# Optimization experiments

Measured on AMD Instinct MI355X. Metric: run time of the kernel, lower is better.

The kernel has to match this reference:

```python
import jax, jax.numpy as jnp
import numpy as np

STATE_DIM = 128
N_RBF = 20
R_CUT = 10.0
N_NODES = 25000
N_EDGES = 250000
N_GRAPHS = 512
N_ATOMS = 100
NUM_ROUNDS = 1


def setup_inputs() -> dict:
    key = jax.random.key(0)
    ks = jax.random.split(key, 20)
    D = STATE_DIM

    def w(k, shape, s=0.05):
        return jax.random.normal(k, shape, jnp.float32) * s

    return {
        "edge_vec": jax.random.normal(ks[0], (N_EDGES, 3), jnp.float32),
        "embedding": w(ks[1], (N_ATOMS, D), 1.0),
        "phi_W1": w(ks[2], (D, D)), "phi_b1": jnp.zeros((D,), jnp.float32),
        "phi_W2": w(ks[3], (D, 3 * D)), "phi_b2": jnp.zeros((3 * D,), jnp.float32),
        "filt_W": w(ks[4], (N_RBF, 3 * D)), "filt_b": jnp.zeros((3 * D,), jnp.float32),
        "upd_W1": w(ks[5], (2 * D, D)), "upd_b1": jnp.zeros((D,), jnp.float32),
        "upd_W2": w(ks[6], (D, 3 * D)), "upd_b2": jnp.zeros((3 * D,), jnp.float32),
        "out_W1": w(ks[7], (D, D)), "out_b1": jnp.zeros((D,), jnp.float32),
        "out_W2": w(ks[8], (D, 1)), "out_b2": jnp.zeros((1,), jnp.float32),
        "U_W": w(ks[9], (D, D)),
        "V_W": w(ks[10], (D, D)),
        "atom_types": jax.random.randint(ks[11], (N_NODES,), 0, N_ATOMS),
        "node_from": jax.random.randint(ks[12], (N_EDGES,), 0, N_NODES),
        "node_to": jax.random.randint(ks[13], (N_EDGES,), 0, N_NODES),
        "node_graph_index": jnp.sort(jax.random.randint(ks[14], (N_NODES,), 0, N_GRAPHS)),
        "num_graphs": N_GRAPHS,
    }


def _painn_forward(edge_vec, embedding, phi_W1, phi_b1, phi_W2, phi_b2,
                   filt_W, filt_b, upd_W1, upd_b1, upd_W2, upd_b2,
                   out_W1, out_b1, out_W2, out_b2, U_W, V_W,
                   atom_types, node_from, node_to, node_graph_index, num_graphs):
    silu = jax.nn.silu
    D = STATE_DIM
    # initial node scalar states from atom-type embedding; vector states zero
    state = embedding[atom_types]                         # [N, D]
    state_vec = jnp.zeros((state.shape[0], 3, D), state.dtype)  # [N, 3, D]

    # edge geometry (constant across rounds)
    d = jnp.linalg.norm(edge_vec, axis=1, keepdims=True)  # [E, 1]
    kfreq = jnp.arange(1, N_RBF + 1, dtype=jnp.float32)   # PaiNN sinc radial basis
    rbf = jnp.sin(kfreq * jnp.pi * d / R_CUT) / d         # [E, n]
    fc = 0.5 * (jnp.cos(jnp.pi * d / R_CUT) + 1.0) * (d < R_CUT)  # cosine cutoff [E,1]
    W_out = (rbf @ filt_W + filt_b) * fc                  # [E, 3D]
    normalized = edge_vec / d                             # [E, 3]

    for _ in range(NUM_ROUNDS):
        # --- message block ---
        inp = state[node_from]                             # gather [E, D]
        phi = silu(inp @ phi_W1 + phi_b1) @ phi_W2 + phi_b2  # [E, 3D]
        pf = phi * W_out                                   # [E, 3D]
        m1, m2, m3 = pf[:, :D], pf[:, D:2 * D], pf[:, 2 * D:]
        msg_vec = (state_vec[node_from] * m1[:, None, :]
                   + normalized[:, :, None] * m3[:, None, :])  # [E, 3, D]
        state = state.at[node_to].add(m2)                  # scatter-add scalars
        state_vec = state_vec.at[node_to].add(msg_vec)     # scatter-add vectors

        # --- update block (torch detaches state_vec here) ---
        sv = jax.lax.stop_gradient(state_vec)
        Up = sv @ U_W                                      # [N, 3, D]
        Vp = sv @ V_W                                      # [N, 3, D]
        UV = jnp.sum(Up * Vp, axis=1)                      # [N, D]
        Vn = jnp.linalg.norm(Vp, axis=1)                   # [N, D]
        h = jnp.concatenate([Vn, state], axis=1)           # [N, 2D]
        a = silu(h @ upd_W1 + upd_b1) @ upd_W2 + upd_b2    # [N, 3D]
        a_vv, a_sv, a_ss = a[:, :D], a[:, D:2 * D], a[:, 2 * D:]
        state = state + a_ss + UV * a_sv
        state_vec = state_vec + Up * a_vv[:, None, :]

    idx = node_graph_index - node_graph_index[0]
    graph_state = jax.ops.segment_sum(state, idx, num_segments=num_graphs)  # [G, D]
    return silu(graph_state @ out_W1 + out_b1) @ out_W2 + out_b2            # [G, 1]


def reference(edge_vec, embedding, phi_W1, phi_b1, phi_W2, phi_b2,
              filt_W, filt_b, upd_W1, upd_b1, upd_W2, upd_b2,
              out_W1, out_b1, out_W2, out_b2, U_W, V_W,
              atom_types, node_from, node_to, node_graph_index, num_graphs):
    return _painn_forward(edge_vec, embedding, phi_W1, phi_b1, phi_W2, phi_b2,
                          filt_W, filt_b, upd_W1, upd_b1, upd_W2, upd_b2,
                          out_W1, out_b1, out_W2, out_b2, U_W, V_W,
                          atom_types, node_from, node_to, node_graph_index, num_graphs)
```

## Files before the change

### kernel.cpp

```cpp
#include <hip/hip_runtime.h>
#include <math.h>

#define D 128
#define NRBF 20
#define NEDGES 250000
#define NNODES 25000
#define NGRAPHS 512
#define NATOMS 100

constexpr float RCUT = 10.0f;
constexpr float PI_F = 3.14159265358979323846f;

__device__ __forceinline__ float silu_f(float x) { return x / (1.0f + __expf(-x)); }

__global__ __launch_bounds__(128) void k_phi_table(
    const float* __restrict__ emb, const float* __restrict__ W1, const float* __restrict__ b1,
    const float* __restrict__ W2, const float* __restrict__ b2, float* __restrict__ phi_tab)
{
    __shared__ float s_in[D];
    __shared__ float s_hid[D];
    const int t = blockIdx.x;
    const int j = threadIdx.x;
    s_in[j] = emb[t * D + j];
    __syncthreads();
    float acc = b1[j];
    for (int c = 0; c < D; ++c) acc = fmaf(s_in[c], W1[c * D + j], acc);
    s_hid[j] = silu_f(acc);
    __syncthreads();
    #pragma unroll
    for (int r = 0; r < 3; ++r) {
        const int col = r * D + j;
        float a2 = b2[col];
        for (int c = 0; c < D; ++c) a2 = fmaf(s_hid[c], W2[c * 384 + col], a2);
        phi_tab[t * 384 + col] = a2;
    }
}

__global__ void k_zero(int* __restrict__ counts, float* __restrict__ gs)
{
    const int i = blockIdx.x * 256 + threadIdx.x;
    if (i < NNODES) counts[i] = 0;
    if (i < NGRAPHS * D) gs[i] = 0.f;
}

__global__ void k_hist(const int* __restrict__ node_to, int* __restrict__ counts)
{
    const int e = blockIdx.x * 256 + threadIdx.x;
    if (e < NEDGES) atomicAdd(&counts[node_to[e]], 1);
}

__global__ __launch_bounds__(1024) void k_scan(int* __restrict__ counts,
                                               int* __restrict__ row_ptr)
{
    __shared__ int s[1024];
    const int t = threadIdx.x;
    const int base = t * 25;
    int sum = 0;
    for (int j = 0; j < 25; ++j) {
        const int idx = base + j;
        if (idx < NNODES) sum += counts[idx];
    }
    s[t] = sum;
    __syncthreads();
    for (int off = 1; off < 1024; off <<= 1) {
        int v = 0;
        if (t >= off) v = s[t - off];
        __syncthreads();
        if (t >= off) s[t] += v;
        __syncthreads();
    }
    int run = (t > 0) ? s[t - 1] : 0;
    for (int j = 0; j < 25; ++j) {
        const int idx = base + j;
        if (idx < NNODES) {
            const int v = counts[idx];
            row_ptr[idx] = run;
            counts[idx] = run;
            run += v;
        }
    }
    if (t == 1023) row_ptr[NNODES] = s[1023];
}

__global__ __launch_bounds__(256) void k_pre(
    const float* __restrict__ edge_vec, const int* __restrict__ node_from,
    const int* __restrict__ node_to, const int* __restrict__ atom_types,
    int* __restrict__ cursor, float* __restrict__ edata, int* __restrict__ ety)
{
    const int e = blockIdx.x * 256 + threadIdx.x;
    if (e >= NEDGES) return;
    const float x = edge_vec[e * 3 + 0];
    const float y = edge_vec[e * 3 + 1];
    const float z = edge_vec[e * 3 + 2];
    const float d = sqrtf(x * x + y * y + z * z);
    const float inv = 1.0f / d;
    const float th = PI_F * d / RCUT;
    const float fc = (d < RCUT) ? 0.5f * (__cosf(th) + 1.0f) : 0.0f;
    const float sc = fc * inv;

    float buf[24];
    #pragma unroll
    for (int k = 0; k < NRBF; ++k) buf[k] = __sinf((float)(k + 1) * th) * sc;
    buf[20] = fc;
    buf[21] = x * inv;
    buf[22] = y * inv;
    buf[23] = z * inv;

    const int slot = atomicAdd(&cursor[node_to[e]], 1);
    float* o = edata + (size_t)slot * 24;
    #pragma unroll
    for (int q = 0; q < 6; ++q) *(float4*)(o + q * 4) = *(float4*)&buf[q * 4];
    ety[slot] = atom_types[node_from[e]];
}

#define GNPB 16
#define CHUNK 64
__global__ __launch_bounds__(256, 4) void k_gather(
    const int* __restrict__ row_ptr, const float* __restrict__ edata,
    const int* __restrict__ ety, const float* __restrict__ phi_tab,
    const float* __restrict__ filt_W, const float* __restrict__ filt_b,
    const float* __restrict__ emb, const int* __restrict__ atom_types,
    float* __restrict__ state, float* __restrict__ sv)
{
    __shared__ __align__(16) float s_ed[CHUNK * 24];
    __shared__ int s_ep[CHUNK];
    __shared__ int s_rp[GNPB + 1];

    const int t = threadIdx.x;
    const bool is_m2 = (t < 128);
    const int lane = t & 127;
    const int c = is_m2 ? (128 + lane) : (256 + lane);

    const int n0 = blockIdx.x * GNPB;
    const int nEnd = min(n0 + GNPB, NNODES);

    if (t <= GNPB) s_rp[t] = row_ptr[min(n0 + t, NNODES)];

    float fw[NRBF];
    #pragma unroll
    for (int k = 0; k < NRBF; ++k) fw[k] = filt_W[k * 384 + c];
    const float fb = filt_b[c];

    __syncthreads();
    const int e0 = s_rp[0];
    const int e1 = s_rp[nEnd - n0];

    int cur = n0;
    int nb = s_rp[1];
    float a0 = 0.f, a1 = 0.f, a2 = 0.f;

    auto do_edge = [&](int j) {
        const float4* p = (const float4*)(s_ed + j * 24);
        const float4 q0 = p[0], q1 = p[1], q2 = p[2], q3 = p[3], q4 = p[4], q5 = p[5];
        const float pt = phi_tab[s_ep[j] * 384 + c];
        float wa = fb * q5.x;
        float wb = q2.z * fw[10];
        wa = fmaf(q0.x, fw[0], wa);  wb = fmaf(q2.w, fw[11], wb);
        wa = fmaf(q0.y, fw[1], wa);  wb = fmaf(q3.x, fw[12], wb);
        wa = fmaf(q0.z, fw[2], wa);  wb = fmaf(q3.y, fw[13], wb);
        wa = fmaf(q0.w, fw[3], wa);  wb = fmaf(q3.z, fw[14], wb);
        wa = fmaf(q1.x, fw[4], wa);  wb = fmaf(q3.w, fw[15], wb);
        wa = fmaf(q1.y, fw[5], wa);  wb = fmaf(q4.x, fw[16], wb);
        wa = fmaf(q1.z, fw[6], wa);  wb = fmaf(q4.y, fw[17], wb);
        wa = fmaf(q1.w, fw[7], wa);  wb = fmaf(q4.z, fw[18], wb);
        wa = fmaf(q2.x, fw[8], wa);  wb = fmaf(q4.w, fw[19], wb);
        wa = fmaf(q2.y, fw[9], wa);
        const float pf = pt * (wa + wb);
        if (is_m2) {
            a0 += pf;
        } else {
            a0 = fmaf(q5.y, pf, a0);
            a1 = fmaf(q5.z, pf, a1);
            a2 = fmaf(q5.w, pf, a2);
        }
    };

    auto flush = [&]() {
        if (is_m2) {
            state[cur * D + lane] = emb[atom_types[cur] * D + lane] + a0;
        } else {
            float* b = sv + (size_t)cur * 3 * D + lane;
            b[0] = a0; b[128] = a1; b[256] = a2;
        }
        a0 = a1 = a2 = 0.f;
        ++cur;
        nb = s_rp[cur - n0 + 1];
    };

    for (int base = e0; base < e1; base += CHUNK) {
        const int cnt = min(CHUNK, e1 - base);
        __syncthreads();
        for (int i = t; i < cnt * 6; i += 256)
            ((float4*)s_ed)[i] = ((const float4*)edata)[(size_t)base * 6 + i];
        for (int i = t; i < cnt; i += 256) s_ep[i] = ety[base + i];
        __syncthreads();

        int j = 0;
        while (j < cnt) {
            while (base + j >= nb) flush();
            const int lim = min(nb - base, cnt);
            #pragma unroll 2
            for (; j < lim; ++j) do_edge(j);
        }
    }
    while (cur < nEnd) flush();
}

#define BNUV 16
__global__ __launch_bounds__(256) void k_uv(
    const float* __restrict__ sv, const float* __restrict__ U_W, const float* __restrict__ V_W,
    float* __restrict__ UVb, float* __restrict__ Vnb)
{
    __shared__ __align__(16) float s_sv[BNUV][3][36];
    __shared__ __align__(16) float s_u[32][128];
    __shared__ __align__(16) float s_v[32][128];
    const int t = threadIdx.x;
    const int cg = t & 15;
    const int ni = t >> 4;
    const int node0 = blockIdx.x * BNUV;

    float up[3][8], vp[3][8];
    #pragma unroll
    for (int a = 0; a < 3; ++a)
        #pragma unroll
        for (int h = 0; h < 8; ++h) { up[a][h] = 0.f; vp[a][h] = 0.f; }

    for (int kt = 0; kt < 4; ++kt) {
        __syncthreads();
        for (int i = t; i < 1024; i += 256) {
            const int row = i >> 5, col = (i & 31) * 4;
            *(float4*)&s_u[row][col] = *(const float4*)(U_W + (kt * 32 + row) * 128 + col);
            *(float4*)&s_v[row][col] = *(const float4*)(V_W + (kt * 32 + row) * 128 + col);
        }
        for (int i = t; i < 384; i += 256) {
            const int nd = i / 24;
            const int rem = i - nd * 24;
            const int a = rem >> 3, c4 = (rem & 7) * 4;
            float4 v = make_float4(0.f, 0.f, 0.f, 0.f);
            if (node0 + nd < NNODES)
                v = *(const float4*)(sv + (size_t)(node0 + nd) * 384 + a * 128 + kt * 32 + c4);
            *(float4*)&s_sv[nd][a][c4] = v;
        }
        __syncthreads();
        #pragma unroll 8
        for (int k = 0; k < 32; ++k) {
            const float xs0 = s_sv[ni][0][k];
            const float xs1 = s_sv[ni][1][k];
            const float xs2 = s_sv[ni][2][k];
            const float4 ua = *(const float4*)&s_u[k][cg * 4];
            const float4 ub = *(const float4*)&s_u[k][64 + cg * 4];
            const float4 va = *(const float4*)&s_v[k][cg * 4];
            const float4 vb = *(const float4*)&s_v[k][64 + cg * 4];
            #define UVSTEP(a, XV) \
                up[a][0] = fmaf(XV, ua.x, up[a][0]); up[a][1] = fmaf(XV, ua.y, up[a][1]); \
                up[a][2] = fmaf(XV, ua.z, up[a][2]); up[a][3] = fmaf(XV, ua.w, up[a][3]); \
                up[a][4] = fmaf(XV, ub.x, up[a][4]); up[a][5] = fmaf(XV, ub.y, up[a][5]); \
                up[a][6] = fmaf(XV, ub.z, up[a][6]); up[a][7] = fmaf(XV, ub.w, up[a][7]); \
                vp[a][0] = fmaf(XV, va.x, vp[a][0]); vp[a][1] = fmaf(XV, va.y, vp[a][1]); \
                vp[a][2] = fmaf(XV, va.z, vp[a][2]); vp[a][3] = fmaf(XV, va.w, vp[a][3]); \
                vp[a][4] = fmaf(XV, vb.x, vp[a][4]); vp[a][5] = fmaf(XV, vb.y, vp[a][5]); \
                vp[a][6] = fmaf(XV, vb.z, vp[a][6]); vp[a][7] = fmaf(XV, vb.w, vp[a][7]);
            UVSTEP(0, xs0) UVSTEP(1, xs1) UVSTEP(2, xs2)
            #undef UVSTEP
        }
    }

    const int n = node0 + ni;
    if (n < NNODES) {
        float uvr[8], vnr[8];
        #pragma unroll
        for (int h = 0; h < 8; ++h) {
            uvr[h] = up[0][h] * vp[0][h] + up[1][h] * vp[1][h] + up[2][h] * vp[2][h];
            vnr[h] = sqrtf(vp[0][h] * vp[0][h] + vp[1][h] * vp[1][h] + vp[2][h] * vp[2][h]);
        }
        float* uo = UVb + n * D;
        float* vo = Vnb + n * D;
        *(float4*)(uo + cg * 4)      = *(float4*)&uvr[0];
        *(float4*)(uo + 64 + cg * 4) = *(float4*)&uvr[4];
        *(float4*)(vo + cg * 4)      = *(float4*)&vnr[0];
        *(float4*)(vo + 64 + cg * 4) = *(float4*)&vnr[4];
    }
}

#define BN1 64
__global__ __launch_bounds__(256) void k_mlp1(
    const float* __restrict__ Vnb, const float* __restrict__ state,
    const float* __restrict__ W1, const float* __restrict__ b1,
    float* __restrict__ hid)
{
    __shared__ __align__(16) float s_h[BN1][36];
    __shared__ __align__(16) float s_w[32][128];
    const int t = threadIdx.x;
    const int cg = t & 15;
    const int rg = t >> 4;
    const int n0 = blockIdx.x * BN1;

    float acc[4][8];
    #pragma unroll
    for (int r = 0; r < 4; ++r)
        #pragma unroll
        for (int h = 0; h < 8; ++h)
            acc[r][h] = (h < 4) ? b1[cg * 4 + h] : b1[64 + cg * 4 + (h - 4)];

    for (int kt = 0; kt < 8; ++kt) {
        const float* src = (kt < 4) ? (Vnb + kt * 32) : (state + (kt - 4) * 32);
        __syncthreads();
        #pragma unroll
        for (int q = 0; q < 2; ++q) {
            const int i = t * 2 + q;
            const int row = i >> 3, c4 = (i & 7) * 4;
            float4 v = make_float4(0.f, 0.f, 0.f, 0.f);
            if (n0 + row < NNODES) v = *(const float4*)(src + (size_t)(n0 + row) * D + c4);
            *(float4*)&s_h[row][c4] = v;
        }
        #pragma unroll
        for (int q = 0; q < 4; ++q) {
            const int i = t + q * 256;
            const int row = i >> 5, col = (i & 31) * 4;
            *(float4*)&s_w[row][col] = *(const float4*)(W1 + (kt * 32 + row) * 128 + col);
        }
        __syncthreads();
        #pragma unroll 8
        for (int k = 0; k < 32; ++k) {
            const float4 wa = *(const float4*)&s_w[k][cg * 4];
            const float4 wb = *(const float4*)&s_w[k][64 + cg * 4];
            #pragma unroll
            for (int r = 0; r < 4; ++r) {
                const float x = s_h[rg * 4 + r][k];
                acc[r][0] = fmaf(x, wa.x, acc[r][0]); acc[r][1] = fmaf(x, wa.y, acc[r][1]);
                acc[r][2] = fmaf(x, wa.z, acc[r][2]); acc[r][3] = fmaf(x, wa.w, acc[r][3]);
                acc[r][4] = fmaf(x, wb.x, acc[r][4]); acc[r][5] = fmaf(x, wb.y, acc[r][5]);
                acc[r][6] = fmaf(x, wb.z, acc[r][6]); acc[r][7] = fmaf(x, wb.w, acc[r][7]);
            }
        }
    }

    #pragma unroll
    for (int r = 0; r < 4; ++r) {
        const int n = n0 + rg * 4 + r;
        if (n < NNODES) {
            float lo[4], hi[4];
            #pragma unroll
            for (int h = 0; h < 4; ++h) { lo[h] = silu_f(acc[r][h]); hi[h] = silu_f(acc[r][h + 4]); }
            *(float4*)(hid + (size_t)n * D + cg * 4)      = *(float4*)lo;
            *(float4*)(hid + (size_t)n * D + 64 + cg * 4) = *(float4*)hi;
        }
    }
}

#define BN2 64
__global__ __launch_bounds__(256) void k_mlp2(
    const float* __restrict__ hid, const float* __restrict__ state,
    const float* __restrict__ UVb,
    const float* __restrict__ W2, const float* __restrict__ b2,
    const int* __restrict__ ngi, float* __restrict__ gs)
{
    __shared__ __align__(16) float s_h[BN2][36];
    __shared__ __align__(16) float s_w2[32][256];
    const int t = threadIdx.x;
    const int cg = t & 15;
    const int rg = t >> 4;
    const int n0 = blockIdx.x * BN2;

    float acc[4][16];
    #pragma unroll
    for (int r = 0; r < 4; ++r)
        #pragma unroll
        for (int g = 0; g < 4; ++g)
            #pragma unroll
            for (int h = 0; h < 4; ++h)
                acc[r][g * 4 + h] = b2[128 + g * 64 + cg * 4 + h];

    for (int kt = 0; kt < 4; ++kt) {
        __syncthreads();
        #pragma unroll
        for (int q = 0; q < 2; ++q) {
            const int i = t * 2 + q;
            const int row = i >> 3, c4 = (i & 7) * 4;
            float4 v = make_float4(0.f, 0.f, 0.f, 0.f);
            if (n0 + row < NNODES)
                v = *(const float4*)(hid + (size_t)(n0 + row) * D + kt * 32 + c4);
            *(float4*)&s_h[row][c4] = v;
        }
        #pragma unroll
        for (int q = 0; q < 8; ++q) {
            const int i = t + q * 256;
            const int row = i >> 6, col = (i & 63) * 4;
            *(float4*)&s_w2[row][col] = *(const float4*)(W2 + (kt * 32 + row) * 384 + 128 + col);
        }
        __syncthreads();
        #pragma unroll 4
        for (int k = 0; k < 32; ++k) {
            const float4 w0 = *(const float4*)&s_w2[k][cg * 4];
            const float4 w1 = *(const float4*)&s_w2[k][64 + cg * 4];
            const float4 w2v = *(const float4*)&s_w2[k][128 + cg * 4];
            const float4 w3 = *(const float4*)&s_w2[k][192 + cg * 4];
            #pragma unroll
            for (int r = 0; r < 4; ++r) {
                const float x = s_h[rg * 4 + r][k];
                acc[r][0]  = fmaf(x, w0.x, acc[r][0]);  acc[r][1]  = fmaf(x, w0.y, acc[r][1]);
                acc[r][2]  = fmaf(x, w0.z, acc[r][2]);  acc[r][3]  = fmaf(x, w0.w, acc[r][3]);
                acc[r][4]  = fmaf(x, w1.x, acc[r][4]);  acc[r][5]  = fmaf(x, w1.y, acc[r][5]);
                acc[r][6]  = fmaf(x, w1.z, acc[r][6]);  acc[r][7]  = fmaf(x, w1.w, acc[r][7]);
                acc[r][8]  = fmaf(x, w2v.x, acc[r][8]); acc[r][9]  = fmaf(x, w2v.y, acc[r][9]);
                acc[r][10] = fmaf(x, w2v.z, acc[r][10]);acc[r][11] = fmaf(x, w2v.w, acc[r][11]);
                acc[r][12] = fmaf(x, w3.x, acc[r][12]); acc[r][13] = fmaf(x, w3.y, acc[r][13]);
                acc[r][14] = fmaf(x, w3.z, acc[r][14]); acc[r][15] = fmaf(x, w3.w, acc[r][15]);
            }
        }
    }

    const int g0 = ngi[0];
    int gprev = -1;
    float run[8];
    #pragma unroll
    for (int r = 0; r < 4; ++r) {
        const int n = n0 + rg * 4 + r;
        if (n >= NNODES) break;
        const int g = ngi[n] - g0;
        const float4 stA = *(const float4*)(state + (size_t)n * D + cg * 4);
        const float4 stB = *(const float4*)(state + (size_t)n * D + 64 + cg * 4);
        const float4 uvA = *(const float4*)(UVb + (size_t)n * D + cg * 4);
        const float4 uvB = *(const float4*)(UVb + (size_t)n * D + 64 + cg * 4);
        float val[8];
        val[0] = stA.x + acc[r][8]  + uvA.x * acc[r][0];
        val[1] = stA.y + acc[r][9]  + uvA.y * acc[r][1];
        val[2] = stA.z + acc[r][10] + uvA.z * acc[r][2];
        val[3] = stA.w + acc[r][11] + uvA.w * acc[r][3];
        val[4] = stB.x + acc[r][12] + uvB.x * acc[r][4];
        val[5] = stB.y + acc[r][13] + uvB.y * acc[r][5];
        val[6] = stB.z + acc[r][14] + uvB.z * acc[r][6];
        val[7] = stB.w + acc[r][15] + uvB.w * acc[r][7];
        if (g == gprev) {
            #pragma unroll
            for (int h = 0; h < 8; ++h) run[h] += val[h];
        } else {
            if (gprev >= 0) {
                float* grow = gs + (size_t)gprev * D;
                #pragma unroll
                for (int h = 0; h < 4; ++h) unsafeAtomicAdd(grow + cg * 4 + h, run[h]);
                #pragma unroll
                for (int h = 0; h < 4; ++h) unsafeAtomicAdd(grow + 64 + cg * 4 + h, run[h + 4]);
            }
            #pragma unroll
            for (int h = 0; h < 8; ++h) run[h] = val[h];
            gprev = g;
        }
    }
    if (gprev >= 0) {
        float* grow = gs + (size_t)gprev * D;
        #pragma unroll
        for (int h = 0; h < 4; ++h) unsafeAtomicAdd(grow + cg * 4 + h, run[h]);
        #pragma unroll
        for (int h = 0; h < 4; ++h) unsafeAtomicAdd(grow + 64 + cg * 4 + h, run[h + 4]);
    }
}

__global__ __launch_bounds__(128) void k_out(
    const float* __restrict__ gs, const float* __restrict__ W1, const float* __restrict__ b1,
    const float* __restrict__ W2, const float* __restrict__ b2, float* __restrict__ out)
{
    __shared__ float s_g[D];
    __shared__ float s_part[2];
    const int g = blockIdx.x;
    const int j = threadIdx.x;
    s_g[j] = gs[g * D + j];
    __syncthreads();
    float acc = b1[j];
    for (int c = 0; c < D; ++c) acc = fmaf(s_g[c], W1[c * D + j], acc);
    float m = silu_f(acc) * W2[j];
    #pragma unroll
    for (int off = 32; off > 0; off >>= 1) m += __shfl_down(m, off);
    if ((j & 63) == 0) s_part[j >> 6] = m;
    __syncthreads();
    if (j == 0) out[g] = s_part[0] + s_part[1] + b2[0];
}

extern "C" void kernel_launch(void* const* d_in, const int* in_sizes, int n_in,
                              void* d_out, int out_size, void* d_ws, size_t ws_size,
                              hipStream_t stream) {
    const float* edge_vec  = (const float*)d_in[0];
    const float* embedding = (const float*)d_in[1];
    const float* phi_W1    = (const float*)d_in[2];
    const float* phi_b1    = (const float*)d_in[3];
    const float* phi_W2    = (const float*)d_in[4];
    const float* phi_b2    = (const float*)d_in[5];
    const float* filt_W    = (const float*)d_in[6];
    const float* filt_b    = (const float*)d_in[7];
    const float* upd_W1    = (const float*)d_in[8];
    const float* upd_b1    = (const float*)d_in[9];
    const float* upd_W2    = (const float*)d_in[10];
    const float* upd_b2    = (const float*)d_in[11];
    const float* out_W1    = (const float*)d_in[12];
    const float* out_b1    = (const float*)d_in[13];
    const float* out_W2    = (const float*)d_in[14];
    const float* out_b2    = (const float*)d_in[15];
    const float* U_W       = (const float*)d_in[16];
    const float* V_W       = (const float*)d_in[17];
    const int* atom_types  = (const int*)d_in[18];
    const int* node_from   = (const int*)d_in[19];
    const int* node_to     = (const int*)d_in[20];
    const int* ngi         = (const int*)d_in[21];
    float* out = (float*)d_out;

    float* ws = (float*)d_ws;
    float* phi_tab = ws;
    float* state   = phi_tab + NATOMS * 384;
    float* sv      = state + NNODES * D;
    float* gsb     = sv + (size_t)NNODES * 3 * D;
    float* scratch = gsb + NGRAPHS * D;
    int*   row_ptr = (int*)scratch;
    int*   counts  = row_ptr + NNODES + 1;
    int*   ety     = counts + NNODES;
    float* edata   = scratch + 300004;
    float* UVb     = scratch;
    float* Vnb     = scratch + NNODES * D;
    float* hid     = sv;

    k_phi_table<<<NATOMS, 128, 0, stream>>>(embedding, phi_W1, phi_b1, phi_W2, phi_b2, phi_tab);
    k_zero<<<(NGRAPHS * D + 255) / 256, 256, 0, stream>>>(counts, gsb);
    k_hist<<<(NEDGES + 255) / 256, 256, 0, stream>>>(node_to, counts);
    k_scan<<<1, 1024, 0, stream>>>(counts, row_ptr);
    k_pre<<<(NEDGES + 255) / 256, 256, 0, stream>>>(
        edge_vec, node_from, node_to, atom_types, counts, edata, ety);
    k_gather<<<(NNODES + GNPB - 1) / GNPB, 256, 0, stream>>>(
        row_ptr, edata, ety, phi_tab, filt_W, filt_b, embedding, atom_types, state, sv);
    k_uv<<<(NNODES + BNUV - 1) / BNUV, 256, 0, stream>>>(sv, U_W, V_W, UVb, Vnb);
    k_mlp1<<<(NNODES + BN1 - 1) / BN1, 256, 0, stream>>>(Vnb, state, upd_W1, upd_b1, hid);
    k_mlp2<<<(NNODES + BN2 - 1) / BN2, 256, 0, stream>>>(hid, state, UVb, upd_W2, upd_b2, ngi, gsb);
    k_out<<<NGRAPHS, 128, 0, stream>>>(gsb, out_W1, out_b1, out_W2, out_b2, out);
}
```

Baseline: 436.3 us.

## Restructure gather, UV, MLP staging and graph pooling kernels

```diff
diff --git a/kernel.cpp b/kernel.cpp
--- a/kernel.cpp
+++ b/kernel.cpp
@@ -36,17 +36,23 @@
     }
 }
 
-__global__ void k_zero(int* __restrict__ counts, float* __restrict__ gs)
+__global__ void k_zero(int* __restrict__ counts, int* __restrict__ glo, int* __restrict__ ghi)
 {
     const int i = blockIdx.x * 256 + threadIdx.x;
     if (i < NNODES) counts[i] = 0;
-    if (i < NGRAPHS * D) gs[i] = 0.f;
-}
-
-__global__ void k_hist(const int* __restrict__ node_to, int* __restrict__ counts)
+    if (i < NGRAPHS) { glo[i] = 0x7fffffff; ghi[i] = -1; }
+}
+
+__global__ void k_hist(const int* __restrict__ node_to, int* __restrict__ counts,
+                       const int* __restrict__ ngi, int* __restrict__ glo, int* __restrict__ ghi)
 {
     const int e = blockIdx.x * 256 + threadIdx.x;
     if (e < NEDGES) atomicAdd(&counts[node_to[e]], 1);
+    if (e < NNODES) {
+        const int g = ngi[e] - ngi[0];
+        atomicMin(&glo[g], e);
+        atomicMax(&ghi[g], e);
+    }
 }
 
 __global__ __launch_bounds__(1024) void k_scan(int* __restrict__ counts,
@@ -115,7 +121,7 @@
 
 #define GNPB 16
 #define CHUNK 64
-__global__ __launch_bounds__(256, 4) void k_gather(
+__global__ __launch_bounds__(128, 4) void k_gather(
     const int* __restrict__ row_ptr, const float* __restrict__ edata,
     const int* __restrict__ ety, const float* __restrict__ phi_tab,
     const float* __restrict__ filt_W, const float* __restrict__ filt_b,
@@ -127,19 +133,21 @@
     __shared__ int s_rp[GNPB + 1];
 
     const int t = threadIdx.x;
-    const bool is_m2 = (t < 128);
-    const int lane = t & 127;
-    const int c = is_m2 ? (128 + lane) : (256 + lane);
+    const int c1 = 128 + t;
+    const int c2 = 256 + t;
 
     const int n0 = blockIdx.x * GNPB;
     const int nEnd = min(n0 + GNPB, NNODES);
-
     if (t <= GNPB) s_rp[t] = row_ptr[min(n0 + t, NNODES)];
 
-    float fw[NRBF];
-    #pragma unroll
-    for (int k = 0; k < NRBF; ++k) fw[k] = filt_W[k * 384 + c];
-    const float fb = filt_b[c];
+    float fw1[NRBF], fw2[NRBF];
+    #pragma unroll
+    for (int k = 0; k < NRBF; ++k) {
+        fw1[k] = filt_W[k * 384 + c1];
+        fw2[k] = filt_W[k * 384 + c2];
+    }
+    const float fb1 = filt_b[c1];
+    const float fb2 = filt_b[c2];
 
     __syncthreads();
     const int e0 = s_rp[0];
@@ -147,42 +155,13 @@
 
     int cur = n0;
     int nb = s_rp[1];
-    float a0 = 0.f, a1 = 0.f, a2 = 0.f;
-
-    auto do_edge = [&](int j) {
-        const float4* p = (const float4*)(s_ed + j * 24);
-        const float4 q0 = p[0], q1 = p[1], q2 = p[2], q3 = p[3], q4 = p[4], q5 = p[5];
-        const float pt = phi_tab[s_ep[j] * 384 + c];
-        float wa = fb * q5.x;
-        float wb = q2.z * fw[10];
-        wa = fmaf(q0.x, fw[0], wa);  wb = fmaf(q2.w, fw[11], wb);
-        wa = fmaf(q0.y, fw[1], wa);  wb = fmaf(q3.x, fw[12], wb);
-        wa = fmaf(q0.z, fw[2], wa);  wb = fmaf(q3.y, fw[13], wb);
-        wa = fmaf(q0.w, fw[3], wa);  wb = fmaf(q3.z, fw[14], wb);
-        wa = fmaf(q1.x, fw[4], wa);  wb = fmaf(q3.w, fw[15], wb);
-        wa = fmaf(q1.y, fw[5], wa);  wb = fmaf(q4.x, fw[16], wb);
-        wa = fmaf(q1.z, fw[6], wa);  wb = fmaf(q4.y, fw[17], wb);
-        wa = fmaf(q1.w, fw[7], wa);  wb = fmaf(q4.z, fw[18], wb);
-        wa = fmaf(q2.x, fw[8], wa);  wb = fmaf(q4.w, fw[19], wb);
-        wa = fmaf(q2.y, fw[9], wa);
-        const float pf = pt * (wa + wb);
-        if (is_m2) {
-            a0 += pf;
-        } else {
-            a0 = fmaf(q5.y, pf, a0);
-            a1 = fmaf(q5.z, pf, a1);
-            a2 = fmaf(q5.w, pf, a2);
-        }
-    };
+    float s0 = 0.f, v0 = 0.f, v1 = 0.f, v2 = 0.f;
 
     auto flush = [&]() {
-        if (is_m2) {
-            state[cur * D + lane] = emb[atom_types[cur] * D + lane] + a0;
-        } else {
-            float* b = sv + (size_t)cur * 3 * D + lane;
-            b[0] = a0; b[128] = a1; b[256] = a2;
-        }
-        a0 = a1 = a2 = 0.f;
+        state[cur * D + t] = emb[atom_types[cur] * D + t] + s0;
+        float* b = sv + (size_t)cur * 3 * D + t;
+        b[0] = v0; b[128] = v1; b[256] = v2;
+        s0 = v0 = v1 = v2 = 0.f;
         ++cur;
         nb = s_rp[cur - n0 + 1];
     };
@@ -190,95 +169,146 @@
     for (int base = e0; base < e1; base += CHUNK) {
         const int cnt = min(CHUNK, e1 - base);
         __syncthreads();
-        for (int i = t; i < cnt * 6; i += 256)
+        for (int i = t; i < cnt * 6; i += 128)
             ((float4*)s_ed)[i] = ((const float4*)edata)[(size_t)base * 6 + i];
-        for (int i = t; i < cnt; i += 256) s_ep[i] = ety[base + i];
+        for (int i = t; i < cnt; i += 128) s_ep[i] = ety[base + i];
         __syncthreads();
 
         int j = 0;
         while (j < cnt) {
             while (base + j >= nb) flush();
             const int lim = min(nb - base, cnt);
+            int ty = s_ep[j];
+            float p1 = phi_tab[ty * 384 + c1];
+            float p2 = phi_tab[ty * 384 + c2];
             #pragma unroll 2
-            for (; j < lim; ++j) do_edge(j);
+            for (; j < lim; ++j) {
+                const float cp1 = p1, cp2 = p2;
+                if (j + 1 < cnt) {
+                    const int tyn = s_ep[j + 1];
+                    p1 = phi_tab[tyn * 384 + c1];
+                    p2 = phi_tab[tyn * 384 + c2];
+                }
+                const float4* p = (const float4*)(s_ed + j * 24);
+                const float4 q0 = p[0], q1 = p[1], q2 = p[2], q3 = p[3], q4 = p[4], q5 = p[5];
+                float wa1 = fb1 * q5.x,      wb1 = q2.z * fw1[10];
+                float wa2 = fb2 * q5.x,      wb2 = q2.z * fw2[10];
+                wa1 = fmaf(q0.x, fw1[0], wa1);  wb1 = fmaf(q2.w, fw1[11], wb1);
+                wa2 = fmaf(q0.x, fw2[0], wa2);  wb2 = fmaf(q2.w, fw2[11], wb2);
+                wa1 = fmaf(q0.y, fw1[1], wa1);  wb1 = fmaf(q3.x, fw1[12], wb1);
+                wa2 = fmaf(q0.y, fw2[1], wa2);  wb2 = fmaf(q3.x, fw2[12], wb2);
+                wa1 = fmaf(q0.z, fw1[2], wa1);  wb1 = fmaf(q3.y, fw1[13], wb1);
+                wa2 = fmaf(q0.z, fw2[2], wa2);  wb2 = fmaf(q3.y, fw2[13], wb2);
+                wa1 = fmaf(q0.w, fw1[3], wa1);  wb1 = fmaf(q3.z, fw1[14], wb1);
+                wa2 = fmaf(q0.w, fw2[3], wa2);  wb2 = fmaf(q3.z, fw2[14], wb2);
+                wa1 = fmaf(q1.x, fw1[4], wa1);  wb1 = fmaf(q3.w, fw1[15], wb1);
+                wa2 = fmaf(q1.x, fw2[4], wa2);  wb2 = fmaf(q3.w, fw2[15], wb2);
+                wa1 = fmaf(q1.y, fw1[5], wa1);  wb1 = fmaf(q4.x, fw1[16], wb1);
+                wa2 = fmaf(q1.y, fw2[5], wa2);  wb2 = fmaf(q4.x, fw2[16], wb2);
+                wa1 = fmaf(q1.z, fw1[6], wa1);  wb1 = fmaf(q4.y, fw1[17], wb1);
+                wa2 = fmaf(q1.z, fw2[6], wa2);  wb2 = fmaf(q4.y, fw2[17], wb2);
+                wa1 = fmaf(q1.w, fw1[7], wa1);  wb1 = fmaf(q4.z, fw1[18], wb1);
+                wa2 = fmaf(q1.w, fw2[7], wa2);  wb2 = fmaf(q4.z, fw2[18], wb2);
+                wa1 = fmaf(q2.x, fw1[8], wa1);  wb1 = fmaf(q4.w, fw1[19], wb1);
+                wa2 = fmaf(q2.x, fw2[8], wa2);  wb2 = fmaf(q4.w, fw2[19], wb2);
+                wa1 = fmaf(q2.y, fw1[9], wa1);
+                wa2 = fmaf(q2.y, fw2[9], wa2);
+                const float pf1 = cp1 * (wa1 + wb1);
+                const float pf2 = cp2 * (wa2 + wb2);
+                s0 += pf1;
+                v0 = fmaf(q5.y, pf2, v0);
+                v1 = fmaf(q5.z, pf2, v1);
+                v2 = fmaf(q5.w, pf2, v2);
+            }
         }
     }
     while (cur < nEnd) flush();
 }
 
-#define BNUV 16
+#define UVBN 64
 __global__ __launch_bounds__(256) void k_uv(
     const float* __restrict__ sv, const float* __restrict__ U_W, const float* __restrict__ V_W,
     float* __restrict__ UVb, float* __restrict__ Vnb)
 {
-    __shared__ __align__(16) float s_sv[BNUV][3][36];
+    __shared__ float s_x[UVBN][33];
     __shared__ __align__(16) float s_u[32][128];
     __shared__ __align__(16) float s_v[32][128];
     const int t = threadIdx.x;
     const int cg = t & 15;
-    const int ni = t >> 4;
-    const int node0 = blockIdx.x * BNUV;
-
-    float up[3][8], vp[3][8];
-    #pragma unroll
-    for (int a = 0; a < 3; ++a)
-        #pragma unroll
-        for (int h = 0; h < 8; ++h) { up[a][h] = 0.f; vp[a][h] = 0.f; }
-
-    for (int kt = 0; kt < 4; ++kt) {
-        __syncthreads();
-        for (int i = t; i < 1024; i += 256) {
-            const int row = i >> 5, col = (i & 31) * 4;
-            *(float4*)&s_u[row][col] = *(const float4*)(U_W + (kt * 32 + row) * 128 + col);
-            *(float4*)&s_v[row][col] = *(const float4*)(V_W + (kt * 32 + row) * 128 + col);
-        }
-        for (int i = t; i < 384; i += 256) {
-            const int nd = i / 24;
-            const int rem = i - nd * 24;
-            const int a = rem >> 3, c4 = (rem & 7) * 4;
-            float4 v = make_float4(0.f, 0.f, 0.f, 0.f);
-            if (node0 + nd < NNODES)
-                v = *(const float4*)(sv + (size_t)(node0 + nd) * 384 + a * 128 + kt * 32 + c4);
-            *(float4*)&s_sv[nd][a][c4] = v;
-        }
-        __syncthreads();
-        #pragma unroll 8
-        for (int k = 0; k < 32; ++k) {
-            const float xs0 = s_sv[ni][0][k];
-            const float xs1 = s_sv[ni][1][k];
-            const float xs2 = s_sv[ni][2][k];
-            const float4 ua = *(const float4*)&s_u[k][cg * 4];
-            const float4 ub = *(const float4*)&s_u[k][64 + cg * 4];
-            const float4 va = *(const float4*)&s_v[k][cg * 4];
-            const float4 vb = *(const float4*)&s_v[k][64 + cg * 4];
-            #define UVSTEP(a, XV) \
-                up[a][0] = fmaf(XV, ua.x, up[a][0]); up[a][1] = fmaf(XV, ua.y, up[a][1]); \
-                up[a][2] = fmaf(XV, ua.z, up[a][2]); up[a][3] = fmaf(XV, ua.w, up[a][3]); \
-                up[a][4] = fmaf(XV, ub.x, up[a][4]); up[a][5] = fmaf(XV, ub.y, up[a][5]); \
-                up[a][6] = fmaf(XV, ub.z, up[a][6]); up[a][7] = fmaf(XV, ub.w, up[a][7]); \
-                vp[a][0] = fmaf(XV, va.x, vp[a][0]); vp[a][1] = fmaf(XV, va.y, vp[a][1]); \
-                vp[a][2] = fmaf(XV, va.z, vp[a][2]); vp[a][3] = fmaf(XV, va.w, vp[a][3]); \
-                vp[a][4] = fmaf(XV, vb.x, vp[a][4]); vp[a][5] = fmaf(XV, vb.y, vp[a][5]); \
-                vp[a][6] = fmaf(XV, vb.z, vp[a][6]); vp[a][7] = fmaf(XV, vb.w, vp[a][7]);
-            UVSTEP(0, xs0) UVSTEP(1, xs1) UVSTEP(2, xs2)
-            #undef UVSTEP
-        }
-    }
-
-    const int n = node0 + ni;
-    if (n < NNODES) {
-        float uvr[8], vnr[8];
-        #pragma unroll
-        for (int h = 0; h < 8; ++h) {
-            uvr[h] = up[0][h] * vp[0][h] + up[1][h] * vp[1][h] + up[2][h] * vp[2][h];
-            vnr[h] = sqrtf(vp[0][h] * vp[0][h] + vp[1][h] * vp[1][h] + vp[2][h] * vp[2][h]);
-        }
-        float* uo = UVb + n * D;
-        float* vo = Vnb + n * D;
-        *(float4*)(uo + cg * 4)      = *(float4*)&uvr[0];
-        *(float4*)(uo + 64 + cg * 4) = *(float4*)&uvr[4];
-        *(float4*)(vo + cg * 4)      = *(float4*)&vnr[0];
-        *(float4*)(vo + 64 + cg * 4) = *(float4*)&vnr[4];
+    const int rg = t >> 4;
+    const int n0 = blockIdx.x * UVBN;
+
+    float uvacc[4][8], vnacc[4][8];
+    #pragma unroll
+    for (int r = 0; r < 4; ++r)
+        #pragma unroll
+        for (int h = 0; h < 8; ++h) { uvacc[r][h] = 0.f; vnacc[r][h] = 0.f; }
+
+    for (int a = 0; a < 3; ++a) {
+        float up[4][8], vp[4][8];
+        #pragma unroll
+        for (int r = 0; r < 4; ++r)
+            #pragma unroll
+            for (int h = 0; h < 8; ++h) { up[r][h] = 0.f; vp[r][h] = 0.f; }
+
+        for (int kt = 0; kt < 4; ++kt) {
+            __syncthreads();
+            for (int i = t; i < UVBN * 32; i += 256) {
+                const int row = i >> 5, col = i & 31;
+                float xv = 0.f;
+                if (n0 + row < NNODES)
+                    xv = sv[(size_t)(n0 + row) * 384 + a * 128 + kt * 32 + col];
+                s_x[row][col] = xv;
+            }
+            #pragma unroll
+            for (int q = 0; q < 4; ++q) {
+                const int i = t + q * 256;
+                const int row = i >> 5, col = (i & 31) * 4;
+                *(float4*)&s_u[row][col] = *(const float4*)(U_W + (kt * 32 + row) * 128 + col);
+                *(float4*)&s_v[row][col] = *(const float4*)(V_W + (kt * 32 + row) * 128 + col);
+            }
+            __syncthreads();
+            #pragma unroll 4
+            for (int k = 0; k < 32; ++k) {
+                const float4 ua = *(const float4*)&s_u[k][cg * 4];
+                const float4 ub = *(const float4*)&s_u[k][64 + cg * 4];
+                const float4 va = *(const float4*)&s_v[k][cg * 4];
+                const float4 vb = *(const float4*)&s_v[k][64 + cg * 4];
+                #pragma unroll
+                for (int r = 0; r < 4; ++r) {
+                    const float x = s_x[rg * 4 + r][k];
+                    up[r][0] = fmaf(x, ua.x, up[r][0]); up[r][1] = fmaf(x, ua.y, up[r][1]);
+                    up[r][2] = fmaf(x, ua.z, up[r][2]); up[r][3] = fmaf(x, ua.w, up[r][3]);
+                    up[r][4] = fmaf(x, ub.x, up[r][4]); up[r][5] = fmaf(x, ub.y, up[r][5]);
+                    up[r][6] = fmaf(x, ub.z, up[r][6]); up[r][7] = fmaf(x, ub.w, up[r][7]);
+                    vp[r][0] = fmaf(x, va.x, vp[r][0]); vp[r][1] = fmaf(x, va.y, vp[r][1]);
+                    vp[r][2] = fmaf(x, va.z, vp[r][2]); vp[r][3] = fmaf(x, va.w, vp[r][3]);
+                    vp[r][4] = fmaf(x, vb.x, vp[r][4]); vp[r][5] = fmaf(x, vb.y, vp[r][5]);
+                    vp[r][6] = fmaf(x, vb.z, vp[r][6]); vp[r][7] = fmaf(x, vb.w, vp[r][7]);
+                }
+            }
+        }
+        #pragma unroll
+        for (int r = 0; r < 4; ++r)
+            #pragma unroll
+            for (int h = 0; h < 8; ++h) {
+                uvacc[r][h] = fmaf(up[r][h], vp[r][h], uvacc[r][h]);
+                vnacc[r][h] = fmaf(vp[r][h], vp[r][h], vnacc[r][h]);
+            }
+    }
+
+    #pragma unroll
+    for (int r = 0; r < 4; ++r) {
+        const int n = n0 + rg * 4 + r;
+        if (n < NNODES) {
+            float vn[8];
+            #pragma unroll
+            for (int h = 0; h < 8; ++h) vn[h] = sqrtf(vnacc[r][h]);
+            *(float4*)(UVb + (size_t)n * D + cg * 4)      = *(float4*)&uvacc[r][0];
+            *(float4*)(UVb + (size_t)n * D + 64 + cg * 4) = *(float4*)&uvacc[r][4];
+            *(float4*)(Vnb + (size_t)n * D + cg * 4)      = *(float4*)&vn[0];
+            *(float4*)(Vnb + (size_t)n * D + 64 + cg * 4) = *(float4*)&vn[4];
+        }
     }
 }
 
@@ -288,7 +318,7 @@
     const float* __restrict__ W1, const float* __restrict__ b1,
     float* __restrict__ hid)
 {
-    __shared__ __align__(16) float s_h[BN1][36];
+    __shared__ float s_h[BN1][33];
     __shared__ __align__(16) float s_w[32][128];
     const int t = threadIdx.x;
     const int cg = t & 15;
@@ -305,13 +335,11 @@
     for (int kt = 0; kt < 8; ++kt) {
         const float* src = (kt < 4) ? (Vnb + kt * 32) : (state + (kt - 4) * 32);
         __syncthreads();
-        #pragma unroll
-        for (int q = 0; q < 2; ++q) {
-            const int i = t * 2 + q;
-            const int row = i >> 3, c4 = (i & 7) * 4;
-            float4 v = make_float4(0.f, 0.f, 0.f, 0.f);
-            if (n0 + row < NNODES) v = *(const float4*)(src + (size_t)(n0 + row) * D + c4);
-            *(float4*)&s_h[row][c4] = v;
+        for (int i = t; i < BN1 * 32; i += 256) {
+            const int row = i >> 5, col = i & 31;
+            float v = 0.f;
+            if (n0 + row < NNODES) v = src[(size_t)(n0 + row) * D + col];
+            s_h[row][col] = v;
         }
         #pragma unroll
         for (int q = 0; q < 4; ++q) {
@@ -353,9 +381,9 @@
     const float* __restrict__ hid, const float* __restrict__ state,
     const float* __restrict__ UVb,
     const float* __restrict__ W2, const float* __restrict__ b2,
-    const int* __restrict__ ngi, float* __restrict__ gs)
-{
-    __shared__ __align__(16) float s_h[BN2][36];
+    float* __restrict__ nodeval)
+{
+    __shared__ float s_h[BN2][33];
     __shared__ __align__(16) float s_w2[32][256];
     const int t = threadIdx.x;
     const int cg = t & 15;
@@ -373,14 +401,11 @@
 
     for (int kt = 0; kt < 4; ++kt) {
         __syncthreads();
-        #pragma unroll
-        for (int q = 0; q < 2; ++q) {
-            const int i = t * 2 + q;
-            const int row = i >> 3, c4 = (i & 7) * 4;
-            float4 v = make_float4(0.f, 0.f, 0.f, 0.f);
-            if (n0 + row < NNODES)
-                v = *(const float4*)(hid + (size_t)(n0 + row) * D + kt * 32 + c4);
-            *(float4*)&s_h[row][c4] = v;
+        for (int i = t; i < BN2 * 32; i += 256) {
+            const int row = i >> 5, col = i & 31;
+            float v = 0.f;
+            if (n0 + row < NNODES) v = hid[(size_t)(n0 + row) * D + kt * 32 + col];
+            s_h[row][col] = v;
         }
         #pragma unroll
         for (int q = 0; q < 8; ++q) {
@@ -410,61 +435,43 @@
         }
     }
 
-    const int g0 = ngi[0];
-    int gprev = -1;
-    float run[8];
     #pragma unroll
     for (int r = 0; r < 4; ++r) {
         const int n = n0 + rg * 4 + r;
         if (n >= NNODES) break;
-        const int g = ngi[n] - g0;
         const float4 stA = *(const float4*)(state + (size_t)n * D + cg * 4);
         const float4 stB = *(const float4*)(state + (size_t)n * D + 64 + cg * 4);
         const float4 uvA = *(const float4*)(UVb + (size_t)n * D + cg * 4);
         const float4 uvB = *(const float4*)(UVb + (size_t)n * D + 64 + cg * 4);
-        float val[8];
-        val[0] = stA.x + acc[r][8]  + uvA.x * acc[r][0];
-        val[1] = stA.y + acc[r][9]  + uvA.y * acc[r][1];
-        val[2] = stA.z + acc[r][10] + uvA.z * acc[r][2];
-        val[3] = stA.w + acc[r][11] + uvA.w * acc[r][3];
-        val[4] = stB.x + acc[r][12] + uvB.x * acc[r][4];
-        val[5] = stB.y + acc[r][13] + uvB.y * acc[r][5];
-        val[6] = stB.z + acc[r][14] + uvB.z * acc[r][6];
-        val[7] = stB.w + acc[r][15] + uvB.w * acc[r][7];
-        if (g == gprev) {
-            #pragma unroll
-            for (int h = 0; h < 8; ++h) run[h] += val[h];
-        } else {
-            if (gprev >= 0) {
-                float* grow = gs + (size_t)gprev * D;
-                #pragma unroll
-                for (int h = 0; h < 4; ++h) unsafeAtomicAdd(grow + cg * 4 + h, run[h]);
-                #pragma unroll
-                for (int h = 0; h < 4; ++h) unsafeAtomicAdd(grow + 64 + cg * 4 + h, run[h + 4]);
-            }
-            #pragma unroll
-            for (int h = 0; h < 8; ++h) run[h] = val[h];
-            gprev = g;
-        }
-    }
-    if (gprev >= 0) {
-        float* grow = gs + (size_t)gprev * D;
-        #pragma unroll
-        for (int h = 0; h < 4; ++h) unsafeAtomicAdd(grow + cg * 4 + h, run[h]);
-        #pragma unroll
-        for (int h = 0; h < 4; ++h) unsafeAtomicAdd(grow + 64 + cg * 4 + h, run[h + 4]);
-    }
-}
-
-__global__ __launch_bounds__(128) void k_out(
-    const float* __restrict__ gs, const float* __restrict__ W1, const float* __restrict__ b1,
+        float va[4], vb[4];
+        va[0] = stA.x + acc[r][8]  + uvA.x * acc[r][0];
+        va[1] = stA.y + acc[r][9]  + uvA.y * acc[r][1];
+        va[2] = stA.z + acc[r][10] + uvA.z * acc[r][2];
+        va[3] = stA.w + acc[r][11] + uvA.w * acc[r][3];
+        vb[0] = stB.x + acc[r][12] + uvB.x * acc[r][4];
+        vb[1] = stB.y + acc[r][13] + uvB.y * acc[r][5];
+        vb[2] = stB.z + acc[r][14] + uvB.z * acc[r][6];
+        vb[3] = stB.w + acc[r][15] + uvB.w * acc[r][7];
+        *(float4*)(nodeval + (size_t)n * D + cg * 4)      = *(float4*)va;
+        *(float4*)(nodeval + (size_t)n * D + 64 + cg * 4) = *(float4*)vb;
+    }
+}
+
+__global__ __launch_bounds__(128) void k_seg_out(
+    const float* __restrict__ nodeval, const int* __restrict__ glo, const int* __restrict__ ghi,
+    const float* __restrict__ W1, const float* __restrict__ b1,
     const float* __restrict__ W2, const float* __restrict__ b2, float* __restrict__ out)
 {
     __shared__ float s_g[D];
     __shared__ float s_part[2];
     const int g = blockIdx.x;
     const int j = threadIdx.x;
-    s_g[j] = gs[g * D + j];
+    const int lo = glo[g];
+    const int hi = ghi[g];
+    float s = 0.f;
+    #pragma unroll 4
+    for (int n = lo; n <= hi; ++n) s += nodeval[(size_t)n * D + j];
+    s_g[j] = s;
     __syncthreads();
     float acc = b1[j];
     for (int c = 0; c < D; ++c) acc = fmaf(s_g[c], W1[c * D + j], acc);
@@ -507,8 +514,10 @@
     float* phi_tab = ws;
     float* state   = phi_tab + NATOMS * 384;
     float* sv      = state + NNODES * D;
-    float* gsb     = sv + (size_t)NNODES * 3 * D;
-    float* scratch = gsb + NGRAPHS * D;
+    float* meta    = sv + (size_t)NNODES * 3 * D;
+    float* scratch = meta + NGRAPHS * D;
+    int*   glo     = (int*)meta;
+    int*   ghi     = glo + NGRAPHS;
     int*   row_ptr = (int*)scratch;
     int*   counts  = row_ptr + NNODES + 1;
     int*   ety     = counts + NNODES;
@@ -516,17 +525,18 @@
     float* UVb     = scratch;
     float* Vnb     = scratch + NNODES * D;
     float* hid     = sv;
+    float* nodeval = sv + NNODES * D;
 
     k_phi_table<<<NATOMS, 128, 0, stream>>>(embedding, phi_W1, phi_b1, phi_W2, phi_b2, phi_tab);
-    k_zero<<<(NGRAPHS * D + 255) / 256, 256, 0, stream>>>(counts, gsb);
-    k_hist<<<(NEDGES + 255) / 256, 256, 0, stream>>>(node_to, counts);
+    k_zero<<<(NNODES + 255) / 256, 256, 0, stream>>>(counts, glo, ghi);
+    k_hist<<<(NEDGES + 255) / 256, 256, 0, stream>>>(node_to, counts, ngi, glo, ghi);
     k_scan<<<1, 1024, 0, stream>>>(counts, row_ptr);
     k_pre<<<(NEDGES + 255) / 256, 256, 0, stream>>>(
         edge_vec, node_from, node_to, atom_types, counts, edata, ety);
-    k_gather<<<(NNODES + GNPB - 1) / GNPB, 256, 0, stream>>>(
+    k_gather<<<(NNODES + GNPB - 1) / GNPB, 128, 0, stream>>>(
         row_ptr, edata, ety, phi_tab, filt_W, filt_b, embedding, atom_types, state, sv);
-    k_uv<<<(NNODES + BNUV - 1) / BNUV, 256, 0, stream>>>(sv, U_W, V_W, UVb, Vnb);
+    k_uv<<<(NNODES + UVBN - 1) / UVBN, 256, 0, stream>>>(sv, U_W, V_W, UVb, Vnb);
     k_mlp1<<<(NNODES + BN1 - 1) / BN1, 256, 0, stream>>>(Vnb, state, upd_W1, upd_b1, hid);
-    k_mlp2<<<(NNODES + BN2 - 1) / BN2, 256, 0, stream>>>(hid, state, UVb, upd_W2, upd_b2, ngi, gsb);
-    k_out<<<NGRAPHS, 128, 0, stream>>>(gsb, out_W1, out_b1, out_W2, out_b2, out);
-}
+    k_mlp2<<<(NNODES + BN2 - 1) / BN2, 256, 0, stream>>>(hid, state, UVb, upd_W2, upd_b2, nodeval);
+    k_seg_out<<<NGRAPHS, 128, 0, stream>>>(nodeval, glo, ghi, out_W1, out_b1, out_W2, out_b2, out);
+}
```

New measurement: 488.6 us. +12.0%, slower.
